# Kernel tuning notes

Hardware: AMD Instinct MI355X
Metric: run time of the kernel (lower is better)

Reference implementation:

```python
import jax, jax.numpy as jnp
import numpy as np

SLOPE = 0.01   # torch LeakyReLU default negative_slope
TASK_TYPE = 2
N, E = 50000, 800000
IN, EMB, OUT, EF = 128, 128, 128, 64


def leaky(x):
    return jnp.where(x >= 0, x, SLOPE * x)


def setup_inputs() -> dict:
    key = jax.random.key(0)
    ks = jax.random.split(key, 12)
    nf = jax.random.normal(ks[0], (N, IN), jnp.float32)
    ef = jax.random.normal(ks[1], (E, EF), jnp.float32)
    src = jax.random.randint(ks[2], (E,), 0, N)
    dst = jax.random.randint(ks[3], (E,), 0, N)
    ntype = jax.random.randint(ks[4], (N,), 0, 4)
    # layer dims: (in, out) per GNNLayer
    dims = [(IN, EMB), (EMB, EMB), (EMB, OUT)]
    inp = {"nf": nf, "ef": ef, "src": src, "dst": dst, "ntype": ntype}
    for i, (di, do) in enumerate(dims):
        inp[f"W_edge_{i}"] = jax.random.normal(ks[5 + i], (2 * di + EF, do), jnp.float32) / np.sqrt(2 * di + EF)
        inp[f"W_node_{i}"] = jax.random.normal(ks[8 + i], (di + do, do), jnp.float32) / np.sqrt(di + do)
    return inp


def gnn_layer(nf, ef, We, Wn, src, dst, active, recv):
    # message: concat(src_nf, dst_nf, ef) -> Linear(no bias) -> LeakyReLU, only on edges from task nodes
    m_in = jnp.concatenate([nf[src], nf[dst], ef], axis=-1)   # [E, 2*di+EF]
    msg = leaky(m_in @ We) * active[:, None]                  # [E, do]
    # reduce: sum messages at destination nodes
    red = jax.ops.segment_sum(msg, dst, num_segments=nf.shape[0])  # [N, do]
    # apply: concat(nf, red_msg) -> Linear(no bias) -> LeakyReLU; only receiving nodes updated (others zero, DGL default)
    out = leaky(jnp.concatenate([nf, red], axis=-1) @ Wn) * recv[:, None]
    return out


def reference(nf, ef, W_edge_0, W_edge_1, W_edge_2, W_node_0, W_node_1, W_node_2, src, dst, ntype):
    active = (ntype[src] == TASK_TYPE).astype(nf.dtype)       # edges emitted by push(u=task_nodes)
    recv = (jax.ops.segment_sum(active, dst, num_segments=nf.shape[0]) > 0).astype(nf.dtype)
    Wes = [W_edge_0, W_edge_1, W_edge_2]
    Wns = [W_node_0, W_node_1, W_node_2]
    h = nf
    for We, Wn in zip(Wes, Wns):
        h = gnn_layer(h, ef, We, Wn, src, dst, active, recv)  # residual=False
    return h
```

## Files before the change

kernel.cpp:

```cpp
#include <hip/hip_runtime.h>

typedef unsigned short u16;
typedef short s16x8 __attribute__((ext_vector_type(8)));
typedef float f32x4 __attribute__((ext_vector_type(4)));

#define SLOPE 0.01f
#define EPB 64

__device__ __forceinline__ float leaky(float x) { return x >= 0.f ? x : SLOPE * x; }

__device__ __forceinline__ u16 f2b(float f) {
    union { float f; unsigned u; } v; v.f = f;
    unsigned r = v.u + 0x7FFFu + ((v.u >> 16) & 1u);
    return (u16)(r >> 16);
}
__device__ __forceinline__ float b2f(u16 b) {
    union { unsigned u; float f; } v; v.u = ((unsigned)b) << 16; return v.f;
}

__global__ __launch_bounds__(256) void k_init(
    const int* __restrict__ src, const int* __restrict__ dst,
    const int* __restrict__ ntype, int* __restrict__ deg,
    float* __restrict__ recvf, int* __restrict__ tflag,
    char* __restrict__ eact, int E, int N)
{
    int i = blockIdx.x * 256 + threadIdx.x;
    if (i < E) {
        bool p = (ntype[src[i]] == 2);
        eact[i] = p ? 1 : 0;
        if (p) {
            int d = dst[i];
            atomicAdd(&deg[d], 1);
            recvf[d] = 1.0f;
        }
    } else {
        int j = i - E;
        if (j < N) tflag[j] = (ntype[j] == 2) ? 1 : 0;
    }
}

__global__ __launch_bounds__(256) void k_scan1(
    const int* __restrict__ deg, const int* __restrict__ tflag,
    int* __restrict__ bsum, int* __restrict__ bsum2, int n)
{
    __shared__ int s[256];
    const int* v = blockIdx.y ? tflag : deg;
    int* out = blockIdx.y ? bsum2 : bsum;
    int i = blockIdx.x * 256 + threadIdx.x;
    s[threadIdx.x] = (i < n) ? v[i] : 0;
    __syncthreads();
    for (int o = 128; o > 0; o >>= 1) {
        if (threadIdx.x < o) s[threadIdx.x] += s[threadIdx.x + o];
        __syncthreads();
    }
    if (threadIdx.x == 0) out[blockIdx.x] = s[0];
}

__global__ __launch_bounds__(256) void k_scan2(
    int* __restrict__ bsum, int* __restrict__ bsum2, int nb,
    int* __restrict__ cntp, int* __restrict__ tcntp)
{
    __shared__ int s[256];
    int* arr = blockIdx.x ? bsum2 : bsum;
    int* tot = blockIdx.x ? tcntp : cntp;
    int v = (threadIdx.x < nb) ? arr[threadIdx.x] : 0;
    s[threadIdx.x] = v;
    __syncthreads();
    for (int o = 1; o < 256; o <<= 1) {
        int x = (threadIdx.x >= o) ? s[threadIdx.x - o] : 0;
        __syncthreads();
        s[threadIdx.x] += x;
        __syncthreads();
    }
    if (threadIdx.x < nb) arr[threadIdx.x] = s[threadIdx.x] - v;
    if (threadIdx.x == 255) *tot = s[255];
}

__global__ __launch_bounds__(256) void k_scan3(
    const int* __restrict__ deg, const int* __restrict__ tflag,
    const int* __restrict__ bsum, const int* __restrict__ bsum2,
    int* __restrict__ cursor, int* __restrict__ trank,
    int* __restrict__ tlist, int n)
{
    __shared__ int s[256];
    const int sel = blockIdx.y;
    const int* v = sel ? tflag : deg;
    const int* bexcl = sel ? bsum2 : bsum;
    int i = blockIdx.x * 256 + threadIdx.x;
    int x = (i < n) ? v[i] : 0;
    s[threadIdx.x] = x;
    __syncthreads();
    for (int o = 1; o < 256; o <<= 1) {
        int y = (threadIdx.x >= o) ? s[threadIdx.x - o] : 0;
        __syncthreads();
        s[threadIdx.x] += y;
        __syncthreads();
    }
    if (i < n) {
        int off = bexcl[blockIdx.x] + s[threadIdx.x] - x;
        if (sel) {
            trank[i] = off;
            if (x) tlist[off] = i;
        } else {
            cursor[i] = off;
        }
    }
}

__global__ __launch_bounds__(256) void k_scatter_pos(
    const int* __restrict__ src, const int* __restrict__ dst,
    const char* __restrict__ eact, const int* __restrict__ trank,
    int* __restrict__ cursor, int* __restrict__ eS,
    int* __restrict__ sSg, int E)
{
    int e = blockIdx.x * 256 + threadIdx.x;
    if (e < E && eact[e]) {
        int d = dst[e];
        int p = atomicAdd(&cursor[d], 1);
        eS[p] = e; sSg[p] = trank[src[e]];
    }
}

__global__ __launch_bounds__(256) void k_prep(
    const float* __restrict__ nf, u16* __restrict__ hb0, int n4,
    const float* __restrict__ We0, const float* __restrict__ We1,
    const float* __restrict__ We2, const float* __restrict__ Wn0,
    const float* __restrict__ Wn1, const float* __restrict__ Wn2,
    u16* __restrict__ WTe, u16* __restrict__ WTn, u16* __restrict__ WTef,
    const float* __restrict__ ef, const int* __restrict__ eS,
    const int* __restrict__ cntp, u16* __restrict__ efS, int E)
{
    int i = blockIdx.x * 256 + threadIdx.x;
    if (i < n4) {
        float4 v = ((const float4*)nf)[i];
        ushort4 o;
        o.x = f2b(v.x); o.y = f2b(v.y); o.z = f2b(v.z); o.w = f2b(v.w);
        ((ushort4*)hb0)[i] = o;
        return;
    }
    int j = i - n4;
    if (j < 3 * 73728) {
        int l = j / 73728;
        int idx = j - l * 73728;
        const float* We = (l == 0) ? We0 : (l == 1) ? We1 : We2;
        const float* Wn = (l == 0) ? Wn0 : (l == 1) ? Wn1 : Wn2;
        if (idx < 32768) {
            int sel = idx >> 14, jj = idx & 16383;
            int k = jj >> 7, n = jj & 127;
            WTe[(size_t)l * 32768 + sel * 16384 + n * 128 + k] = f2b(We[sel * 16384 + jj]);
        } else if (idx < 65536) {
            int jj = idx - 32768;
            int k = jj >> 7, n = jj & 127;
            WTn[(size_t)l * 32768 + n * 256 + k] = f2b(Wn[jj]);
        } else {
            int jj = idx - 65536;
            int k = jj >> 7, n = jj & 127;
            WTef[(size_t)l * 8192 + n * 64 + k] = f2b(We[32768 + jj]);
        }
        return;
    }
    int g = j - 3 * 73728;
    if (g >= E * 16) return;
    int p = g >> 4, f4 = g & 15;
    if (p < *cntp) {
        float4 v = *(const float4*)(ef + (size_t)eS[p] * 64 + f4 * 4);
        ushort4 o;
        o.x = f2b(v.x); o.y = f2b(v.y); o.z = f2b(v.z); o.w = f2b(v.w);
        *(ushort4*)(efS + (size_t)p * 64 + f4 * 4) = o;
    }
}

__global__ __launch_bounds__(256) void k_T2msg(
    const u16* __restrict__ A, const u16* __restrict__ WTe_l,
    u16* __restrict__ Tsrc, u16* __restrict__ Tdst,
    const int* __restrict__ tlist, const int* __restrict__ tcntp,
    const u16* __restrict__ efS, const u16* __restrict__ WTef_l,
    const int* __restrict__ cntp, u16* __restrict__ msgS,
    int Nfull, int nT64)
{
    __shared__ u16 sh[64 * 72 + 128 * 72];
    const int t = threadIdx.x;
    const int bx = blockIdx.x;
    const int w = t >> 6, lane = t & 63;
    const int lo = lane & 15, q = lane >> 4;

    if (bx < 2 * nT64) {
        u16 (*As)[72] = (u16(*)[72])sh;
        u16 (*Bs)[72] = (u16(*)[72])(sh + 64 * 72);
        const int sel = (bx >= nT64) ? 1 : 0;
        const int M = sel ? Nfull : *tcntp;
        const int m0 = (bx - sel * nT64) * 64;
        if (m0 >= M) return;
        const u16* WT = WTe_l + sel * 16384;
        u16* T = sel ? Tdst : Tsrc;
        const int wm = w >> 1, wn = w & 1;
        f32x4 acc[2][4] = {};

        for (int kt = 0; kt < 128; kt += 64) {
            #pragma unroll
            for (int p = 0; p < 2; ++p) {
                int c = t + p * 256;
                int row = c >> 3, k8 = c & 7;
                int gm = m0 + row;
                int4 va = make_int4(0, 0, 0, 0);
                if (gm < M) {
                    int arow = sel ? gm : tlist[gm];
                    va = *(const int4*)(A + (size_t)arow * 128 + kt + k8 * 8);
                }
                *(int4*)&As[row][k8 * 8] = va;
            }
            #pragma unroll
            for (int p = 0; p < 4; ++p) {
                int c = t + p * 256;
                int row = c >> 3, k8 = c & 7;
                *(int4*)&Bs[row][k8 * 8] =
                    *(const int4*)(WT + (size_t)row * 128 + kt + k8 * 8);
            }
            __syncthreads();
            #pragma unroll
            for (int kf = 0; kf < 2; ++kf) {
                s16x8 a[2], b[4];
                #pragma unroll
                for (int mi = 0; mi < 2; ++mi)
                    a[mi] = *(const s16x8*)&As[wm * 32 + mi * 16 + lo][kf * 32 + q * 8];
                #pragma unroll
                for (int ni = 0; ni < 4; ++ni)
                    b[ni] = *(const s16x8*)&Bs[wn * 64 + ni * 16 + lo][kf * 32 + q * 8];
                #pragma unroll
                for (int mi = 0; mi < 2; ++mi)
                    #pragma unroll
                    for (int ni = 0; ni < 4; ++ni)
                        acc[mi][ni] = __builtin_amdgcn_mfma_f32_16x16x32_bf16(
                            a[mi], b[ni], acc[mi][ni], 0, 0, 0);
            }
            __syncthreads();
        }
        #pragma unroll
        for (int mi = 0; mi < 2; ++mi) {
            #pragma unroll
            for (int r = 0; r < 4; ++r) {
                int gm = m0 + wm * 32 + mi * 16 + q * 4 + r;
                if (gm < M) {
                    #pragma unroll
                    for (int ni = 0; ni < 4; ++ni)
                        T[(size_t)gm * 128 + wn * 64 + ni * 16 + lo] = f2b(acc[mi][ni][r]);
                }
            }
        }
    } else {
        u16 (*Ms)[136] = (u16(*)[136])sh;
        const int cnt = *cntp;
        const int b0 = (bx - 2 * nT64) * EPB;
        if (b0 >= cnt) return;
        const int ei = w * 16 + lo;
        const int p = b0 + ei;

        f32x4 acc[8] = {};
        #pragma unroll
        for (int kf = 0; kf < 2; ++kf) {
            s16x8 b = {};
            if (p < cnt) b = *(const s16x8*)(efS + (size_t)p * 64 + kf * 32 + q * 8);
            #pragma unroll
            for (int mi = 0; mi < 8; ++mi) {
                s16x8 a = *(const s16x8*)(WTef_l + (size_t)(mi * 16 + lo) * 64 + kf * 32 + q * 8);
                acc[mi] = __builtin_amdgcn_mfma_f32_16x16x32_bf16(a, b, acc[mi], 0, 0, 0);
            }
        }
        #pragma unroll
        for (int mi = 0; mi < 8; ++mi) {
            ushort4 o;
            o.x = f2b(acc[mi][0]); o.y = f2b(acc[mi][1]);
            o.z = f2b(acc[mi][2]); o.w = f2b(acc[mi][3]);
            *(ushort4*)&Ms[ei][mi * 16 + q * 4] = o;
        }
        __syncthreads();
        #pragma unroll
        for (int pz = 0; pz < 4; ++pz) {
            int idx = t + pz * 256;
            int rrow = idx >> 4, c8 = idx & 15;
            int pp = b0 + rrow;
            if (pp < cnt)
                *(int4*)(msgS + (size_t)pp * 128 + c8 * 8) = *(const int4*)&Ms[rrow][c8 * 8];
        }
    }
}

__global__ __launch_bounds__(256) void k_reduce(
    const u16* __restrict__ msgS, const u16* __restrict__ Tsrc,
    const u16* __restrict__ Tdst, const int* __restrict__ sSg,
    const int* __restrict__ deg, const int* __restrict__ segEnd,
    u16* __restrict__ redb, int N)
{
    const int w = threadIdx.x >> 6, lane = threadIdx.x & 63;
    const int d = blockIdx.x * 4 + w;
    if (d >= N) return;
    const int dg = deg[d];
    if (dg == 0) return;
    const int end = segEnd[d], beg = end - dg;

    unsigned td = *(const unsigned*)(Tdst + (size_t)d * 128 + lane * 2);
    const float td0 = b2f((u16)(td & 0xffff)), td1 = b2f((u16)(td >> 16));
    float a0 = 0.f, a1 = 0.f;
    for (int i = beg; i < end; ++i) {
        int s = sSg[i];
        unsigned m  = *(const unsigned*)(msgS + (size_t)i * 128 + lane * 2);
        unsigned ts = *(const unsigned*)(Tsrc + (size_t)s * 128 + lane * 2);
        a0 += leaky(b2f((u16)(m & 0xffff)) + b2f((u16)(ts & 0xffff)) + td0);
        a1 += leaky(b2f((u16)(m >> 16))    + b2f((u16)(ts >> 16))    + td1);
    }
    unsigned out = (unsigned)f2b(a0) | ((unsigned)f2b(a1) << 16);
    *(unsigned*)(redb + (size_t)d * 128 + lane * 2) = out;
}

__global__ __launch_bounds__(256) void k_gemm_node(
    const u16* __restrict__ H, const u16* __restrict__ R,
    const u16* __restrict__ WT, const float* __restrict__ recvf,
    u16* __restrict__ O16, float* __restrict__ O32, int fin, int M)
{
    __shared__ u16 As[64][72];
    __shared__ u16 Bs[128][72];
    const int t = threadIdx.x;
    const int m0 = blockIdx.x * 64;
    if (m0 >= M) return;
    const int w = t >> 6, lane = t & 63;
    const int lo = lane & 15, q = lane >> 4;
    const int wm = w >> 1, wn = w & 1;
    f32x4 acc[2][4] = {};

    for (int kt = 0; kt < 256; kt += 64) {
        const u16* Ap = (kt < 128) ? (H + kt) : (R + (kt - 128));
        #pragma unroll
        for (int p = 0; p < 2; ++p) {
            int c = t + p * 256;
            int row = c >> 3, k8 = c & 7;
            int gm = m0 + row;
            int4 va = make_int4(0, 0, 0, 0);
            if (gm < M) va = *(const int4*)(Ap + (size_t)gm * 128 + k8 * 8);
            *(int4*)&As[row][k8 * 8] = va;
        }
        #pragma unroll
        for (int p = 0; p < 4; ++p) {
            int c = t + p * 256;
            int row = c >> 3, k8 = c & 7;
            *(int4*)&Bs[row][k8 * 8] =
                *(const int4*)(WT + (size_t)row * 256 + kt + k8 * 8);
        }
        __syncthreads();
        #pragma unroll
        for (int kf = 0; kf < 2; ++kf) {
            s16x8 a[2], b[4];
            #pragma unroll
            for (int mi = 0; mi < 2; ++mi)
                a[mi] = *(const s16x8*)&As[wm * 32 + mi * 16 + lo][kf * 32 + q * 8];
            #pragma unroll
            for (int ni = 0; ni < 4; ++ni)
                b[ni] = *(const s16x8*)&Bs[wn * 64 + ni * 16 + lo][kf * 32 + q * 8];
            #pragma unroll
            for (int mi = 0; mi < 2; ++mi)
                #pragma unroll
                for (int ni = 0; ni < 4; ++ni)
                    acc[mi][ni] = __builtin_amdgcn_mfma_f32_16x16x32_bf16(
                        a[mi], b[ni], acc[mi][ni], 0, 0, 0);
        }
        __syncthreads();
    }
    #pragma unroll
    for (int mi = 0; mi < 2; ++mi) {
        #pragma unroll
        for (int r = 0; r < 4; ++r) {
            int gm = m0 + wm * 32 + mi * 16 + q * 4 + r;
            if (gm < M) {
                float rv = recvf[gm];
                #pragma unroll
                for (int ni = 0; ni < 4; ++ni) {
                    float val = leaky(acc[mi][ni][r]) * rv;
                    size_t o = (size_t)gm * 128 + wn * 64 + ni * 16 + lo;
                    if (fin) O32[o] = val;
                    else     O16[o] = f2b(val);
                }
            }
        }
    }
}

extern "C" void kernel_launch(void* const* d_in, const int* in_sizes, int n_in,
                              void* d_out, int out_size, void* d_ws, size_t ws_size,
                              hipStream_t stream)
{
    const float* nf    = (const float*)d_in[0];
    const float* ef    = (const float*)d_in[1];
    const int*   src   = (const int*)d_in[2];
    const int*   dst   = (const int*)d_in[3];
    const int*   ntype = (const int*)d_in[4];
    const float* We[3] = {(const float*)d_in[5], (const float*)d_in[7], (const float*)d_in[9]};
    const float* Wn[3] = {(const float*)d_in[6], (const float*)d_in[8], (const float*)d_in[10]};

    const int N = in_sizes[0] / 128;
    const int E = in_sizes[1] / 64;

    u16* Tsrc = (u16*)d_ws;
    u16* Tdst = Tsrc + (size_t)N * 128;
    u16* hb0  = Tdst + (size_t)N * 128;
    u16* hb1  = hb0 + (size_t)N * 128;
    u16* redb = hb1 + (size_t)N * 128;
    u16* WTe  = redb + (size_t)N * 128;
    u16* WTn  = WTe + 3 * 32768;
    u16* WTef = WTn + 3 * 32768;
    u16* efS  = WTef + 3 * 8192;
    u16* msgS = efS + (size_t)E * 64;
    float* recvf = (float*)(msgS + (size_t)E * 128);
    int* deg    = (int*)(recvf + N);
    int* cursor = deg + N;
    int* tflag  = cursor + N;
    int* trank  = tflag + N;
    int* tlist  = trank + N;
    int* bsum   = tlist + N;
    int* bsum2  = bsum + 256;
    int* cntp   = bsum2 + 256;
    int* tcntp  = cntp + 4;
    int* eS     = tcntp + 4;
    int* sSg    = eS + E;
    char* eact  = (char*)(sSg + E);

    const int nb  = (N + 255) / 256;
    const int gEb = (E + 255) / 256;
    const int n4  = N * 128 / 4;
    const int nT64 = (N + 63) / 64;
    const int gM  = (E + EPB - 1) / EPB;
    const int prepWork = n4 + 3 * 73728 + E * 16;

    hipMemsetAsync(recvf, 0, (size_t)N * 2 * sizeof(float), stream);

    k_init<<<(E + N + 255) / 256, 256, 0, stream>>>(src, dst, ntype, deg, recvf, tflag, eact, E, N);
    k_scan1<<<dim3(nb, 2), 256, 0, stream>>>(deg, tflag, bsum, bsum2, N);
    k_scan2<<<2, 256, 0, stream>>>(bsum, bsum2, nb, cntp, tcntp);
    k_scan3<<<dim3(nb, 2), 256, 0, stream>>>(deg, tflag, bsum, bsum2, cursor, trank, tlist, N);
    k_scatter_pos<<<gEb, 256, 0, stream>>>(src, dst, eact, trank, cursor, eS, sSg, E);
    k_prep<<<(prepWork + 255) / 256, 256, 0, stream>>>(
        nf, hb0, n4, We[0], We[1], We[2], Wn[0], Wn[1], Wn[2], WTe, WTn, WTef,
        ef, eS, cntp, efS, E);

    int gR = (N + 3) / 4;

    const u16* hIn[3]  = {hb0, hb1, hb0};
    u16*       hOut[3] = {hb1, hb0, hb1};
    for (int l = 0; l < 3; ++l) {
        int fin = (l == 2);
        k_T2msg<<<2 * nT64 + gM, 256, 0, stream>>>(
            hIn[l], WTe + (size_t)l * 32768, Tsrc, Tdst, tlist, tcntp,
            efS, WTef + (size_t)l * 8192, cntp, msgS, N, nT64);
        k_reduce<<<gR, 256, 0, stream>>>(msgS, Tsrc, Tdst, sSg, deg, cursor, redb, N);
        k_gemm_node<<<nT64, 256, 0, stream>>>(hIn[l], redb, WTn + (size_t)l * 32768,
                                              recvf, hOut[l], (float*)d_out, fin, N);
    }
}
```

Baseline: 315.9 us.

## Merge preprocessing kernels, pack edge-source pairs, and grid-stride message tiles

Folds the init, node-feature conversion and weight transpose work into one kernel, and merges scan2 and scan3 so each block rescans the block sums itself. recvf is now derived from deg during scan1, and the edge-feature gather moves to its own grid-stride kernel bounded by the active edge count. Edge ids and source ranks are packed into one int2 array. The message GEMM now runs a fixed grid that loops over tiles instead of launching one block per possible edge tile, most of which exited early. This cuts launches, the memset and idle blocks, at the cost of redundant block-sum scans and the int2 load in the reduce loop.

```diff
diff --git a/kernel.cpp b/kernel.cpp
--- a/kernel.cpp
+++ b/kernel.cpp
@@ -6,6 +6,7 @@
 
 #define SLOPE 0.01f
 #define EPB 64
+#define MSGB 2048
 
 __device__ __forceinline__ float leaky(float x) { return x >= 0.f ? x : SLOPE * x; }
 
@@ -21,116 +22,24 @@
 __global__ __launch_bounds__(256) void k_init(
     const int* __restrict__ src, const int* __restrict__ dst,
     const int* __restrict__ ntype, int* __restrict__ deg,
-    float* __restrict__ recvf, int* __restrict__ tflag,
-    char* __restrict__ eact, int E, int N)
-{
-    int i = blockIdx.x * 256 + threadIdx.x;
-    if (i < E) {
-        bool p = (ntype[src[i]] == 2);
-        eact[i] = p ? 1 : 0;
-        if (p) {
-            int d = dst[i];
-            atomicAdd(&deg[d], 1);
-            recvf[d] = 1.0f;
-        }
-    } else {
-        int j = i - E;
-        if (j < N) tflag[j] = (ntype[j] == 2) ? 1 : 0;
-    }
-}
-
-__global__ __launch_bounds__(256) void k_scan1(
-    const int* __restrict__ deg, const int* __restrict__ tflag,
-    int* __restrict__ bsum, int* __restrict__ bsum2, int n)
-{
-    __shared__ int s[256];
-    const int* v = blockIdx.y ? tflag : deg;
-    int* out = blockIdx.y ? bsum2 : bsum;
-    int i = blockIdx.x * 256 + threadIdx.x;
-    s[threadIdx.x] = (i < n) ? v[i] : 0;
-    __syncthreads();
-    for (int o = 128; o > 0; o >>= 1) {
-        if (threadIdx.x < o) s[threadIdx.x] += s[threadIdx.x + o];
-        __syncthreads();
-    }
-    if (threadIdx.x == 0) out[blockIdx.x] = s[0];
-}
-
-__global__ __launch_bounds__(256) void k_scan2(
-    int* __restrict__ bsum, int* __restrict__ bsum2, int nb,
-    int* __restrict__ cntp, int* __restrict__ tcntp)
-{
-    __shared__ int s[256];
-    int* arr = blockIdx.x ? bsum2 : bsum;
-    int* tot = blockIdx.x ? tcntp : cntp;
-    int v = (threadIdx.x < nb) ? arr[threadIdx.x] : 0;
-    s[threadIdx.x] = v;
-    __syncthreads();
-    for (int o = 1; o < 256; o <<= 1) {
-        int x = (threadIdx.x >= o) ? s[threadIdx.x - o] : 0;
-        __syncthreads();
-        s[threadIdx.x] += x;
-        __syncthreads();
-    }
-    if (threadIdx.x < nb) arr[threadIdx.x] = s[threadIdx.x] - v;
-    if (threadIdx.x == 255) *tot = s[255];
-}
-
-__global__ __launch_bounds__(256) void k_scan3(
-    const int* __restrict__ deg, const int* __restrict__ tflag,
-    const int* __restrict__ bsum, const int* __restrict__ bsum2,
-    int* __restrict__ cursor, int* __restrict__ trank,
-    int* __restrict__ tlist, int n)
-{
-    __shared__ int s[256];
-    const int sel = blockIdx.y;
-    const int* v = sel ? tflag : deg;
-    const int* bexcl = sel ? bsum2 : bsum;
-    int i = blockIdx.x * 256 + threadIdx.x;
-    int x = (i < n) ? v[i] : 0;
-    s[threadIdx.x] = x;
-    __syncthreads();
-    for (int o = 1; o < 256; o <<= 1) {
-        int y = (threadIdx.x >= o) ? s[threadIdx.x - o] : 0;
-        __syncthreads();
-        s[threadIdx.x] += y;
-        __syncthreads();
-    }
-    if (i < n) {
-        int off = bexcl[blockIdx.x] + s[threadIdx.x] - x;
-        if (sel) {
-            trank[i] = off;
-            if (x) tlist[off] = i;
-        } else {
-            cursor[i] = off;
-        }
-    }
-}
-
-__global__ __launch_bounds__(256) void k_scatter_pos(
-    const int* __restrict__ src, const int* __restrict__ dst,
-    const char* __restrict__ eact, const int* __restrict__ trank,
-    int* __restrict__ cursor, int* __restrict__ eS,
-    int* __restrict__ sSg, int E)
-{
-    int e = blockIdx.x * 256 + threadIdx.x;
-    if (e < E && eact[e]) {
-        int d = dst[e];
-        int p = atomicAdd(&cursor[d], 1);
-        eS[p] = e; sSg[p] = trank[src[e]];
-    }
-}
-
-__global__ __launch_bounds__(256) void k_prep(
+    int* __restrict__ tflag, char* __restrict__ eact,
     const float* __restrict__ nf, u16* __restrict__ hb0, int n4,
     const float* __restrict__ We0, const float* __restrict__ We1,
     const float* __restrict__ We2, const float* __restrict__ Wn0,
     const float* __restrict__ Wn1, const float* __restrict__ Wn2,
     u16* __restrict__ WTe, u16* __restrict__ WTn, u16* __restrict__ WTef,
-    const float* __restrict__ ef, const int* __restrict__ eS,
-    const int* __restrict__ cntp, u16* __restrict__ efS, int E)
+    int E, int N)
 {
     int i = blockIdx.x * 256 + threadIdx.x;
+    if (i < E) {
+        bool p = (ntype[src[i]] == 2);
+        eact[i] = p ? 1 : 0;
+        if (p) atomicAdd(&deg[dst[i]], 1);
+        return;
+    }
+    i -= E;
+    if (i < N) { tflag[i] = (ntype[i] == 2) ? 1 : 0; return; }
+    i -= N;
     if (i < n4) {
         float4 v = ((const float4*)nf)[i];
         ushort4 o;
@@ -139,31 +48,117 @@
         return;
     }
     int j = i - n4;
-    if (j < 3 * 73728) {
-        int l = j / 73728;
-        int idx = j - l * 73728;
-        const float* We = (l == 0) ? We0 : (l == 1) ? We1 : We2;
-        const float* Wn = (l == 0) ? Wn0 : (l == 1) ? Wn1 : Wn2;
-        if (idx < 32768) {
-            int sel = idx >> 14, jj = idx & 16383;
-            int k = jj >> 7, n = jj & 127;
-            WTe[(size_t)l * 32768 + sel * 16384 + n * 128 + k] = f2b(We[sel * 16384 + jj]);
-        } else if (idx < 65536) {
-            int jj = idx - 32768;
-            int k = jj >> 7, n = jj & 127;
-            WTn[(size_t)l * 32768 + n * 256 + k] = f2b(Wn[jj]);
+    if (j >= 3 * 73728) return;
+    int l = j / 73728;
+    int idx = j - l * 73728;
+    const float* We = (l == 0) ? We0 : (l == 1) ? We1 : We2;
+    const float* Wn = (l == 0) ? Wn0 : (l == 1) ? Wn1 : Wn2;
+    if (idx < 32768) {
+        int sel = idx >> 14, jj = idx & 16383;
+        int k = jj >> 7, n = jj & 127;
+        WTe[(size_t)l * 32768 + sel * 16384 + n * 128 + k] = f2b(We[sel * 16384 + jj]);
+    } else if (idx < 65536) {
+        int jj = idx - 32768;
+        int k = jj >> 7, n = jj & 127;
+        WTn[(size_t)l * 32768 + n * 256 + k] = f2b(Wn[jj]);
+    } else {
+        int jj = idx - 65536;
+        int k = jj >> 7, n = jj & 127;
+        WTef[(size_t)l * 8192 + n * 64 + k] = f2b(We[32768 + jj]);
+    }
+}
+
+__global__ __launch_bounds__(256) void k_scan1(
+    const int* __restrict__ deg, const int* __restrict__ tflag,
+    int* __restrict__ bsum, int* __restrict__ bsum2,
+    float* __restrict__ recvf, int n)
+{
+    __shared__ int s[256];
+    const int sel = blockIdx.y;
+    const int* v = sel ? tflag : deg;
+    int* out = sel ? bsum2 : bsum;
+    int i = blockIdx.x * 256 + threadIdx.x;
+    int x = (i < n) ? v[i] : 0;
+    if (!sel && i < n) recvf[i] = (x > 0) ? 1.0f : 0.0f;
+    s[threadIdx.x] = x;
+    __syncthreads();
+    for (int o = 128; o > 0; o >>= 1) {
+        if (threadIdx.x < o) s[threadIdx.x] += s[threadIdx.x + o];
+        __syncthreads();
+    }
+    if (threadIdx.x == 0) out[blockIdx.x] = s[0];
+}
+
+__global__ __launch_bounds__(256) void k_scan23(
+    const int* __restrict__ deg, const int* __restrict__ tflag,
+    const int* __restrict__ bsum, const int* __restrict__ bsum2,
+    int* __restrict__ cursor, int* __restrict__ trank,
+    int* __restrict__ tlist, int* __restrict__ cntp, int* __restrict__ tcntp,
+    int n, int nb)
+{
+    __shared__ int bscan[256];
+    __shared__ int s[256];
+    const int sel = blockIdx.y;
+    const int* v = sel ? tflag : deg;
+    const int* bs = sel ? bsum2 : bsum;
+    const int t = threadIdx.x;
+
+    int bv = (t < nb) ? bs[t] : 0;
+    bscan[t] = bv;
+    __syncthreads();
+    for (int o = 1; o < 256; o <<= 1) {
+        int x = (t >= o) ? bscan[t - o] : 0;
+        __syncthreads();
+        bscan[t] += x;
+        __syncthreads();
+    }
+    const int base  = (blockIdx.x > 0) ? bscan[blockIdx.x - 1] : 0;
+    const int total = bscan[nb - 1];
+
+    int i = blockIdx.x * 256 + t;
+    int x = (i < n) ? v[i] : 0;
+    s[t] = x;
+    __syncthreads();
+    for (int o = 1; o < 256; o <<= 1) {
+        int y = (t >= o) ? s[t - o] : 0;
+        __syncthreads();
+        s[t] += y;
+        __syncthreads();
+    }
+    if (i < n) {
+        int off = base + s[t] - x;
+        if (sel) {
+            trank[i] = off;
+            if (x) tlist[off] = i;
         } else {
-            int jj = idx - 65536;
-            int k = jj >> 7, n = jj & 127;
-            WTef[(size_t)l * 8192 + n * 64 + k] = f2b(We[32768 + jj]);
-        }
-        return;
-    }
-    int g = j - 3 * 73728;
-    if (g >= E * 16) return;
-    int p = g >> 4, f4 = g & 15;
-    if (p < *cntp) {
-        float4 v = *(const float4*)(ef + (size_t)eS[p] * 64 + f4 * 4);
+            cursor[i] = off;
+        }
+    }
+    if (blockIdx.x == 0 && t == 0) *(sel ? tcntp : cntp) = total;
+}
+
+__global__ __launch_bounds__(256) void k_scatter_pos(
+    const int* __restrict__ src, const int* __restrict__ dst,
+    const char* __restrict__ eact, const int* __restrict__ trank,
+    int* __restrict__ cursor, int2* __restrict__ esPair, int E)
+{
+    int e = blockIdx.x * 256 + threadIdx.x;
+    if (e < E && eact[e]) {
+        int d = dst[e];
+        int p = atomicAdd(&cursor[d], 1);
+        esPair[p] = make_int2(e, trank[src[e]]);
+    }
+}
+
+__global__ __launch_bounds__(256) void k_efg(
+    const float* __restrict__ ef, const int2* __restrict__ esPair,
+    const int* __restrict__ cntp, u16* __restrict__ efS)
+{
+    const int chunks = (*cntp) * 16;
+    const int stride = gridDim.x * 256;
+    for (int c = blockIdx.x * 256 + threadIdx.x; c < chunks; c += stride) {
+        int p = c >> 4, f4 = c & 15;
+        float4 v = *(const float4*)(ef + (size_t)esPair[p].x * 64 + f4 * 4);
         ushort4 o;
         o.x = f2b(v.x); o.y = f2b(v.y); o.z = f2b(v.z); o.w = f2b(v.w);
         *(ushort4*)(efS + (size_t)p * 64 + f4 * 4) = o;
@@ -250,44 +245,46 @@
     } else {
         u16 (*Ms)[136] = (u16(*)[136])sh;
         const int cnt = *cntp;
-        const int b0 = (bx - 2 * nT64) * EPB;
-        if (b0 >= cnt) return;
         const int ei = w * 16 + lo;
-        const int p = b0 + ei;
-
-        f32x4 acc[8] = {};
-        #pragma unroll
-        for (int kf = 0; kf < 2; ++kf) {
-            s16x8 b = {};
-            if (p < cnt) b = *(const s16x8*)(efS + (size_t)p * 64 + kf * 32 + q * 8);
+        for (int tile = bx - 2 * nT64; tile * EPB < cnt; tile += MSGB) {
+            const int b0 = tile * EPB;
+            const int p = b0 + ei;
+
+            f32x4 acc[8] = {};
+            #pragma unroll
+            for (int kf = 0; kf < 2; ++kf) {
+                s16x8 b = {};
+                if (p < cnt) b = *(const s16x8*)(efS + (size_t)p * 64 + kf * 32 + q * 8);
+                #pragma unroll
+                for (int mi = 0; mi < 8; ++mi) {
+                    s16x8 a = *(const s16x8*)(WTef_l + (size_t)(mi * 16 + lo) * 64 + kf * 32 + q * 8);
+                    acc[mi] = __builtin_amdgcn_mfma_f32_16x16x32_bf16(a, b, acc[mi], 0, 0, 0);
+                }
+            }
             #pragma unroll
             for (int mi = 0; mi < 8; ++mi) {
-                s16x8 a = *(const s16x8*)(WTef_l + (size_t)(mi * 16 + lo) * 64 + kf * 32 + q * 8);
-                acc[mi] = __builtin_amdgcn_mfma_f32_16x16x32_bf16(a, b, acc[mi], 0, 0, 0);
-            }
-        }
-        #pragma unroll
-        for (int mi = 0; mi < 8; ++mi) {
-            ushort4 o;
-            o.x = f2b(acc[mi][0]); o.y = f2b(acc[mi][1]);
-            o.z = f2b(acc[mi][2]); o.w = f2b(acc[mi][3]);
-            *(ushort4*)&Ms[ei][mi * 16 + q * 4] = o;
-        }
-        __syncthreads();
-        #pragma unroll
-        for (int pz = 0; pz < 4; ++pz) {
-            int idx = t + pz * 256;
-            int rrow = idx >> 4, c8 = idx & 15;
-            int pp = b0 + rrow;
-            if (pp < cnt)
-                *(int4*)(msgS + (size_t)pp * 128 + c8 * 8) = *(const int4*)&Ms[rrow][c8 * 8];
+                ushort4 o;
+                o.x = f2b(acc[mi][0]); o.y = f2b(acc[mi][1]);
+                o.z = f2b(acc[mi][2]); o.w = f2b(acc[mi][3]);
+                *(ushort4*)&Ms[ei][mi * 16 + q * 4] = o;
+            }
+            __syncthreads();
+            #pragma unroll
+            for (int pz = 0; pz < 4; ++pz) {
+                int idx = t + pz * 256;
+                int rrow = idx >> 4, c8 = idx & 15;
+                int pp = b0 + rrow;
+                if (pp < cnt)
+                    *(int4*)(msgS + (size_t)pp * 128 + c8 * 8) = *(const int4*)&Ms[rrow][c8 * 8];
+            }
+            __syncthreads();
         }
     }
 }
 
 __global__ __launch_bounds__(256) void k_reduce(
     const u16* __restrict__ msgS, const u16* __restrict__ Tsrc,
-    const u16* __restrict__ Tdst, const int* __restrict__ sSg,
+    const u16* __restrict__ Tdst, const int2* __restrict__ esPair,
     const int* __restrict__ deg, const int* __restrict__ segEnd,
     u16* __restrict__ redb, int N)
 {
@@ -302,7 +299,7 @@
     const float td0 = b2f((u16)(td & 0xffff)), td1 = b2f((u16)(td >> 16));
     float a0 = 0.f, a1 = 0.f;
     for (int i = beg; i < end; ++i) {
-        int s = sSg[i];
+        int s = esPair[i].y;
         unsigned m  = *(const unsigned*)(msgS + (size_t)i * 128 + lane * 2);
         unsigned ts = *(const unsigned*)(Tsrc + (size_t)s * 128 + lane * 2);
         a0 += leaky(b2f((u16)(m & 0xffff)) + b2f((u16)(ts & 0xffff)) + td0);
@@ -418,27 +415,24 @@
     int* bsum2  = bsum + 256;
     int* cntp   = bsum2 + 256;
     int* tcntp  = cntp + 4;
-    int* eS     = tcntp + 4;
-    int* sSg    = eS + E;
-    char* eact  = (char*)(sSg + E);
+    int2* esPair = (int2*)(tcntp + 4);
+    char* eact  = (char*)(esPair + E);
 
     const int nb  = (N + 255) / 256;
     const int gEb = (E + 255) / 256;
     const int n4  = N * 128 / 4;
     const int nT64 = (N + 63) / 64;
-    const int gM  = (E + EPB - 1) / EPB;
-    const int prepWork = n4 + 3 * 73728 + E * 16;
-
-    hipMemsetAsync(recvf, 0, (size_t)N * 2 * sizeof(float), stream);
-
-    k_init<<<(E + N + 255) / 256, 256, 0, stream>>>(src, dst, ntype, deg, recvf, tflag, eact, E, N);
-    k_scan1<<<dim3(nb, 2), 256, 0, stream>>>(deg, tflag, bsum, bsum2, N);
-    k_scan2<<<2, 256, 0, stream>>>(bsum, bsum2, nb, cntp, tcntp);
-    k_scan3<<<dim3(nb, 2), 256, 0, stream>>>(deg, tflag, bsum, bsum2, cursor, trank, tlist, N);
-    k_scatter_pos<<<gEb, 256, 0, stream>>>(src, dst, eact, trank, cursor, eS, sSg, E);
-    k_prep<<<(prepWork + 255) / 256, 256, 0, stream>>>(
-        nf, hb0, n4, We[0], We[1], We[2], Wn[0], Wn[1], Wn[2], WTe, WTn, WTef,
-        ef, eS, cntp, efS, E);
+    const int initWork = E + N + n4 + 3 * 73728;
+
+    hipMemsetAsync(deg, 0, (size_t)N * sizeof(int), stream);
+    k_init<<<(initWork + 255) / 256, 256, 0, stream>>>(
+        src, dst, ntype, deg, tflag, eact, nf, hb0, n4,
+        We[0], We[1], We[2], Wn[0], Wn[1], Wn[2], WTe, WTn, WTef, E, N);
+    k_scan1<<<dim3(nb, 2), 256, 0, stream>>>(deg, tflag, bsum, bsum2, recvf, N);
+    k_scan23<<<dim3(nb, 2), 256, 0, stream>>>(deg, tflag, bsum, bsum2,
+                                              cursor, trank, tlist, cntp, tcntp, N, nb);
+    k_scatter_pos<<<gEb, 256, 0, stream>>>(src, dst, eact, trank, cursor, esPair, E);
+    k_efg<<<1024, 256, 0, stream>>>(ef, esPair, cntp, efS);
 
     int gR = (N + 3) / 4;
 
@@ -446,10 +440,10 @@
     u16*       hOut[3] = {hb1, hb0, hb1};
     for (int l = 0; l < 3; ++l) {
         int fin = (l == 2);
-        k_T2msg<<<2 * nT64 + gM, 256, 0, stream>>>(
+        k_T2msg<<<2 * nT64 + MSGB, 256, 0, stream>>>(
             hIn[l], WTe + (size_t)l * 32768, Tsrc, Tdst, tlist, tcntp,
             efS, WTef + (size_t)l * 8192, cntp, msgS, N, nT64);
-        k_reduce<<<gR, 256, 0, stream>>>(msgS, Tsrc, Tdst, sSg, deg, cursor, redb, N);
+        k_reduce<<<gR, 256, 0, stream>>>(msgS, Tsrc, Tdst, esPair, deg, cursor, redb, N);
         k_gemm_node<<<nT64, 256, 0, stream>>>(hIn[l], redb, WTn + (size_t)l * 32768,
                                               recvf, hOut[l], (float*)d_out, fin, N);
     }
```

Result: faster. 299.0 us (-5.3%).
